# Kernel tuning notes

Measured on AMD Instinct MI355X. Metric: run time of the kernel, lower is better.

The kernel has to match this reference:

```python
import jax, jax.numpy as jnp
import numpy as np

N_USER = 100_000
N_WALLET = 100_000
E = 1_600_000
HID, OUT = 128, 64
H, C = 4, 32  # GAT heads, per-head channels (HID // 4)
U_IN, W_IN = 16, 4
EPS = 1e-5


def _sage(x_src, x_dst, ei, w_l, b_l, w_r):
    """PyG SAGEConv (mean aggr): lin_l(mean_j x_j) + lin_r(x_i)."""
    src, dst = ei[0], ei[1]
    n = x_dst.shape[0]
    s = jax.ops.segment_sum(x_src[src], dst, num_segments=n)
    deg = jax.ops.segment_sum(jnp.ones((src.shape[0],), x_src.dtype), dst, num_segments=n)
    agg = s / jnp.maximum(deg, 1.0)[:, None]
    return agg @ w_l + b_l + x_dst @ w_r


def _bn(x, g, b):
    """BatchNorm over node dim (training-mode batch stats)."""
    m = x.mean(0)
    v = x.var(0)
    return (x - m) * jax.lax.rsqrt(v + EPS) * g + b


def _segment_softmax(logits, seg, n):
    m = jax.ops.segment_max(logits, seg, num_segments=n)
    e = jnp.exp(logits - m[seg])
    s = jax.ops.segment_sum(e, seg, num_segments=n)
    return e / (s[seg] + 1e-16)


def _gat(x, ei, w, a_src, a_dst, bias):
    """PyG GATConv with self-loops, heads concatenated. Dropout off (eval)."""
    n = x.shape[0]
    loop = jnp.arange(n, dtype=ei.dtype)
    src = jnp.concatenate([ei[0], loop])
    dst = jnp.concatenate([ei[1], loop])
    xp = (x @ w).reshape(n, H, C)                      # [n,H,C]
    al_s = (xp * a_src).sum(-1)                        # [n,H]
    al_d = (xp * a_dst).sum(-1)                        # [n,H]
    logits = jax.nn.leaky_relu(al_s[src] + al_d[dst], 0.2)  # [E+n,H]
    alpha = _segment_softmax(logits, dst, n)
    out = jax.ops.segment_sum(xp[src] * alpha[:, :, None], dst, num_segments=n)
    return out.reshape(n, H * C) + bias


def setup_inputs() -> dict:
    key = jax.random.key(0)
    ks = jax.random.split(key, 24)
    rn = lambda k, s, sc=0.05: jax.random.normal(k, s, jnp.float32) * sc
    ei = lambda k, n: jax.random.randint(k, (2, E), 0, n, jnp.int32)
    return {
        "x_user": rn(ks[0], (N_USER, U_IN), 1.0),
        "x_wallet": rn(ks[1], (N_WALLET, W_IN), 1.0),
        "w_u2w_l": rn(ks[2], (U_IN, HID)), "b_u2w": jnp.zeros((HID,), jnp.float32), "w_u2w_r": rn(ks[3], (W_IN, HID)),
        "w_w2u_l": rn(ks[4], (W_IN, HID)), "b_w2u": jnp.zeros((HID,), jnp.float32), "w_w2u_r": rn(ks[5], (U_IN, HID)),
        "w_u2u_l": rn(ks[6], (U_IN, HID)), "b_u2u": jnp.zeros((HID,), jnp.float32), "w_u2u_r": rn(ks[7], (U_IN, HID)),
        "bn_u_g": jnp.ones((HID,), jnp.float32), "bn_u_b": jnp.zeros((HID,), jnp.float32),
        "bn_w_g": jnp.ones((HID,), jnp.float32), "bn_w_b": jnp.zeros((HID,), jnp.float32),
        "gat_w": rn(ks[8], (HID, H * C)), "gat_as": rn(ks[9], (H, C)), "gat_ad": rn(ks[10], (H, C)),
        "gat_b": jnp.zeros((HID,), jnp.float32),
        "bn2_g": jnp.ones((HID,), jnp.float32), "bn2_b": jnp.zeros((HID,), jnp.float32),
        "proj_w": rn(ks[11], (HID, OUT)), "proj_b": jnp.zeros((OUT,), jnp.float32),
        "ei_uw": ei(ks[12], N_USER),   # src user -> dst wallet (both 100k)
        "ei_wu": ei(ks[13], N_WALLET),  # src wallet -> dst user
        "ei_uu": ei(ks[14], N_USER),
    }


def reference(x_user, x_wallet, w_u2w_l, b_u2w, w_u2w_r, w_w2u_l, b_w2u, w_w2u_r,
              w_u2u_l, b_u2u, w_u2u_r, bn_u_g, bn_u_b, bn_w_g, bn_w_b,
              gat_w, gat_as, gat_ad, gat_b, bn2_g, bn2_b, proj_w, proj_b,
              ei_uw, ei_wu, ei_uu):
    h_w_from_u = jax.nn.relu(_sage(x_user, x_wallet, ei_uw, w_u2w_l, b_u2w, w_u2w_r))
    h_u_from_w = jax.nn.relu(_sage(x_wallet, x_user, ei_wu, w_w2u_l, b_w2u, w_w2u_r))
    h_u_from_u = jax.nn.relu(_sage(x_user, x_user, ei_uu, w_u2u_l, b_u2u, w_u2u_r))
    h_user = _bn(h_u_from_w + h_u_from_u, bn_u_g, bn_u_b)
    _ = _bn(h_w_from_u, bn_w_g, bn_w_b)  # h_wallet: computed in torch module but unused in output
    h_user = jax.nn.relu(_gat(h_user, ei_uu, gat_w, gat_as, gat_ad, gat_b))
    h_user = _bn(h_user, bn2_g, bn2_b)
    return jax.nn.relu(h_user @ proj_w + proj_b)  # dropout = identity (eval)
```

## Files before the change

### kernel.cpp

```cpp
#include <hip/hip_runtime.h>
#include <hip/hip_bf16.h>
#include <cstdint>
#include <cstddef>

#define NN   100000
#define NE   1600000
#define CAP  48

#define NBKT 784
#define BSH  7
#define FB   16
#define BCAP 2432
#define ACHUNK 8192
#define NABLK 196

#define NTILES 1563
#define CH_BN 50
#define NSHAD 4
#define LOG2E 1.44269504088896f

typedef __attribute__((ext_vector_type(8))) short short8;
typedef __attribute__((ext_vector_type(4))) float floatx4;

__device__ inline short f2bs(float x) {
    __hip_bfloat16 h = __float2bfloat16(x);
    return *reinterpret_cast<short*>(&h);
}
__device__ inline int pack2(float a, float b) {
    return ((int)(unsigned short)f2bs(b) << 16) | (unsigned short)f2bs(a);
}
__device__ inline float bflo(unsigned p) { return __uint_as_float(p << 16); }
__device__ inline float bfhi(unsigned p) { return __uint_as_float(p & 0xFFFF0000u); }

#define OFF_PRE   ((size_t)0)
#define OFF_BKTU  ((size_t)0)
#define OFF_BKTW  ((size_t)1906688)
#define OFF_XP    ((size_t)12800000)
#define OFF_AGGU  ((size_t)12800000)
#define OFF_AGGW  ((size_t)14400000)
#define OFF_COLU  ((size_t)19200000)
#define OFF_S1    ((size_t)24000000)
#define OFF_Q1    ((size_t)24000512)
#define OFF_S2    ((size_t)24001024)
#define OFF_Q2    ((size_t)24001536)
#define OFF_BCUR  ((size_t)24002048)
#define OFF_CNTU  ((size_t)25600000)
#define OFF_ALS   ((size_t)25802112)
#define OFF_ALD   ((size_t)26202112)
#define ZBASE     OFF_S1
#define ZFLOATS   ((size_t)3648)

__global__ void __launch_bounds__(256) bin_edges(
    const int* __restrict__ ei_u, const int* __restrict__ ei_w,
    int* __restrict__ bcur_u, int* __restrict__ bkt_u,
    int* __restrict__ bcur_w, int* __restrict__ bkt_w) {
    const int* ei = blockIdx.y ? ei_w : ei_u;
    int* bcur = blockIdx.y ? bcur_w : bcur_u;
    int* bkt  = blockIdx.y ? bkt_w  : bkt_u;
    __shared__ int lcnt[NBKT];
    __shared__ int lbuf[NBKT * FB];
    for (int i = threadIdx.x; i < NBKT; i += 256) lcnt[i] = 0;
    __syncthreads();
    int base = blockIdx.x * ACHUNK;
    #pragma unroll 4
    for (int k = 0; k < ACHUNK / 256; k++) {
        int e = base + k * 256 + threadIdx.x;
        if (e < NE) {
            int src = ei[e], dst = ei[NE + e];
            int b = dst >> BSH;
            int pk = ((dst & ((1 << BSH) - 1)) << 17) | src;
            int pos = atomicAdd(&lcnt[b], 1);
            if (pos < FB) lbuf[b * FB + pos] = pk;
            else {
                int g = atomicAdd(&bcur[b], 1);
                if (g < BCAP) bkt[(size_t)b * BCAP + g] = pk;
            }
        }
    }
    __syncthreads();
    int wid = threadIdx.x >> 6, lane = threadIdx.x & 63;
    const int BPW = NBKT / 4;
    int b0w = wid * BPW;
    for (int r = 0; r < BPW; r += 64) {
        int rb = r + lane;
        if (rb < BPW) {
            int b = b0w + rb;
            int c = lcnt[b];
            int nn2 = c < FB ? c : FB;
            if (nn2 > 0) {
                int g0 = atomicAdd(&bcur[b], nn2);
                for (int i2 = 0; i2 < nn2; i2++) {
                    int g = g0 + i2;
                    if (g < BCAP) bkt[(size_t)b * BCAP + g] = lbuf[b * FB + i2];
                }
            }
        }
    }
}

__global__ void __launch_bounds__(256) csr_agg(
    const int* __restrict__ bcur_u, const int* __restrict__ bkt_u,
    int* __restrict__ cnt_g, int* __restrict__ col_g,
    const float* __restrict__ xu, float* __restrict__ aggu,
    const int* __restrict__ bcur_w, const int* __restrict__ bkt_w,
    const float* __restrict__ xw, float* __restrict__ aggw) {
    int type = blockIdx.y;
    const int* bcur = type ? bcur_w : bcur_u;
    const int* bkt  = type ? bkt_w  : bkt_u;
    int B = blockIdx.x;
    int node_base = B << BSH;
    if (node_base >= NN) return;
    __shared__ int cnt[128];
    __shared__ int col[128 * CAP];
    if (threadIdx.x < 128) cnt[threadIdx.x] = 0;
    __syncthreads();
    int n = bcur[B]; if (n > BCAP) n = BCAP;
    const int* bp = bkt + (size_t)B * BCAP;
    for (int i = threadIdx.x; i < n; i += 256) {
        int p = bp[i];
        int d = p >> 17;
        int pos = atomicAdd(&cnt[d], 1);
        if (pos < CAP) col[d * CAP + pos] = p & 0x1FFFF;
    }
    __syncthreads();
    int nn_here = NN - node_base; if (nn_here > 128) nn_here = 128;
    int wv = threadIdx.x >> 6, lane = threadIdx.x & 63;

    if (type == 0) {
        if (threadIdx.x < nn_here) cnt_g[node_base + threadIdx.x] = cnt[threadIdx.x];
        int total4 = nn_here * CAP / 4;
        const int4* cs = (const int4*)col;
        int4* cg = (int4*)(col_g + (size_t)node_base * CAP);
        for (int i = threadIdx.x; i < total4; i += 256) cg[i] = cs[i];
        int kq = lane & 3, nd = (lane >> 2) & 3, sl = lane >> 4;
        const float4* xu4 = (const float4*)xu;
        for (int nb = wv * 32; nb < wv * 32 + 32; nb += 4) {
            int myn = nb + nd;
            int deg = cnt[myn];
            int nu = deg < CAP ? deg : CAP;
            int numax = nu;
            numax = max(numax, __shfl_xor(numax, 4, 64));
            numax = max(numax, __shfl_xor(numax, 8, 64));
            int iters2 = (numax + 7) >> 3;
            float4 v = make_float4(0.f, 0.f, 0.f, 0.f);
            for (int it = 0; it < iters2; it++) {
                int b0 = sl + (it << 3);
                int b1 = b0 + 4;
                int s0 = (b0 < nu) ? col[myn * CAP + b0] : 0;
                int s1 = (b1 < nu) ? col[myn * CAP + b1] : 0;
                float4 x0 = xu4[(size_t)s0 * 4 + kq];
                float4 x1 = xu4[(size_t)s1 * 4 + kq];
                if (b0 < nu) { v.x += x0.x; v.y += x0.y; v.z += x0.z; v.w += x0.w; }
                if (b1 < nu) { v.x += x1.x; v.y += x1.y; v.z += x1.z; v.w += x1.w; }
            }
            v.x += __shfl_xor(v.x, 16, 64); v.y += __shfl_xor(v.y, 16, 64);
            v.z += __shfl_xor(v.z, 16, 64); v.w += __shfl_xor(v.w, 16, 64);
            v.x += __shfl_xor(v.x, 32, 64); v.y += __shfl_xor(v.y, 32, 64);
            v.z += __shfl_xor(v.z, 32, 64); v.w += __shfl_xor(v.w, 32, 64);
            if (lane < 16) {
                int wn = nb + (lane >> 2);
                if (wn < nn_here) {
                    float r = 1.f / fmaxf((float)cnt[wn], 1.f);
                    float4 o = make_float4(v.x * r, v.y * r, v.z * r, v.w * r);
                    *(float4*)&aggu[(size_t)(node_base + wn) * 16 + 4 * (lane & 3)] = o;
                }
            }
        }
    } else {
        const float4* xw4 = (const float4*)xw;
        for (int nl = wv * 32; nl < wv * 32 + 32; nl += 2) {
            if (nl >= nn_here) break;
            int degA = cnt[nl];
            int degB = (nl + 1 < nn_here) ? cnt[nl + 1] : 0;
            int nwA = degA < CAP ? degA : CAP;
            int nwB = degB < CAP ? degB : CAP;
            int sA = (lane < nwA) ? col[nl * CAP + lane] : 0;
            int sB = (lane < nwB) ? col[(nl + 1) * CAP + lane] : 0;
            float4 xA = xw4[sA];
            float4 xB = xw4[sB];
            float4 vA = (lane < nwA) ? xA : make_float4(0.f, 0.f, 0.f, 0.f);
            float4 vB = (lane < nwB) ? xB : make_float4(0.f, 0.f, 0.f, 0.f);
            #pragma unroll
            for (int m = 1; m <= 32; m <<= 1) {
                vA.x += __shfl_xor(vA.x, m, 64); vA.y += __shfl_xor(vA.y, m, 64);
                vA.z += __shfl_xor(vA.z, m, 64); vA.w += __shfl_xor(vA.w, m, 64);
                vB.x += __shfl_xor(vB.x, m, 64); vB.y += __shfl_xor(vB.y, m, 64);
                vB.z += __shfl_xor(vB.z, m, 64); vB.w += __shfl_xor(vB.w, m, 64);
            }
            if (lane == 0) {
                float rA = 1.f / fmaxf((float)degA, 1.f);
                float4 oA = make_float4(vA.x * rA, vA.y * rA, vA.z * rA, vA.w * rA);
                *(float4*)&aggw[(size_t)(node_base + nl) * 4] = oA;
                if (nl + 1 < nn_here) {
                    float rB = 1.f / fmaxf((float)degB, 1.f);
                    float4 oB = make_float4(vB.x * rB, vB.y * rB, vB.z * rB, vB.w * rB);
                    *(float4*)&aggw[(size_t)(node_base + nl + 1) * 4] = oB;
                }
            }
        }
    }
}

__global__ void __launch_bounds__(256, 2) sage_gemm(
    const float* __restrict__ aggu, const float* __restrict__ aggw,
    const float* __restrict__ xu,
    const float* __restrict__ wl_w2u, const float* __restrict__ b_w2u, const float* __restrict__ wr_w2u,
    const float* __restrict__ wl_u2u, const float* __restrict__ b_u2u, const float* __restrict__ wr_u2u,
    __hip_bfloat16* __restrict__ pre,
    float* __restrict__ bnsum, float* __restrict__ bnsq) {
    __shared__ short lw[16 * 64 * 8];
    __shared__ short la[64 * 136];
    __shared__ float lbs[128], lbq[128];
    int tid = threadIdx.x;
    for (int idx = tid; idx < 8192; idx += 256) {
        int mat = idx >> 12;
        int k = (idx >> 7) & 31, n = idx & 127;
        float w;
        if (mat == 0)
            w = (k < 4) ? wl_w2u[k * 128 + n] : (k < 20 ? wr_w2u[(k - 4) * 128 + n] : 0.f);
        else
            w = (k < 16) ? wl_u2u[k * 128 + n] : wr_u2u[(k - 16) * 128 + n];
        int t = n >> 4, l15 = n & 15, q = (k >> 3) & 3, j = k & 7;
        lw[((mat * 8 + t) * 64 + q * 16 + l15) * 8 + j] = f2bs(w);
    }
    if (tid < 128) { lbs[tid] = 0.f; lbq[tid] = 0.f; }
    __syncthreads();
    int wv = tid >> 6, lane = tid & 63;
    int quad = lane >> 4, l15 = lane & 15;
    short8 w1[8], w2[8];
    #pragma unroll
    for (int t = 0; t < 8; t++) {
        w1[t] = *(const short8*)&lw[(t * 64 + lane) * 8];
        w2[t] = *(const short8*)&lw[((8 + t) * 64 + lane) * 8];
    }
    float bw[8], bu[8];
    #pragma unroll
    for (int t = 0; t < 8; t++) {
        bw[t] = b_w2u[t * 16 + l15];
        bu[t] = b_u2u[t * 16 + l15];
    }
    float sE[8], qE[8];
    #pragma unroll
    for (int t = 0; t < 8; t++) { sE[t] = 0.f; qE[t] = 0.f; }
    for (int tile = blockIdx.x; tile < NTILES; tile += gridDim.x) {
        int nbase = tile * 64;
        __syncthreads();
        {
            int node = tid >> 2, p = tid & 3;
            int gn = nbase + node;
            float4 v = make_float4(0.f, 0.f, 0.f, 0.f);
            if (gn < NN) v = *(const float4*)&xu[(size_t)gn * 16 + 4 * p];
            int2 pk; pk.x = pack2(v.x, v.y); pk.y = pack2(v.z, v.w);
            *(int2*)&la[node * 136 + 4 + 4 * p] = pk;
            *(int2*)&la[node * 136 + 48 + 4 * p] = pk;
        }
        {
            int node = tid >> 2, p = tid & 3;
            int gn = nbase + node;
            float4 v = make_float4(0.f, 0.f, 0.f, 0.f);
            if (gn < NN) v = *(const float4*)&aggu[(size_t)gn * 16 + 4 * p];
            int2 pk; pk.x = pack2(v.x, v.y); pk.y = pack2(v.z, v.w);
            *(int2*)&la[node * 136 + 32 + 4 * p] = pk;
        }
        if (tid < 64) {
            int node = tid, gn = nbase + node;
            float4 v = make_float4(0.f, 0.f, 0.f, 0.f);
            if (gn < NN) v = *(const float4*)&aggw[(size_t)gn * 4];
            int2 pk; pk.x = pack2(v.x, v.y); pk.y = pack2(v.z, v.w);
            *(int2*)&la[node * 136 + 0] = pk;
            int2 z; z.x = 0; z.y = 0;
            *(int2*)&la[node * 136 + 20] = z;
            *(int2*)&la[node * 136 + 24] = z;
            *(int2*)&la[node * 136 + 28] = z;
        }
        __syncthreads();
        short8 af1 = *(const short8*)&la[(wv * 16 + l15) * 136 + quad * 8];
        short8 af2 = *(const short8*)&la[(wv * 16 + l15) * 136 + 32 + quad * 8];
        floatx4 acc1[8], acc2[8];
        #pragma unroll
        for (int t = 0; t < 8; t++) {
            acc1[t] = (floatx4){0.f, 0.f, 0.f, 0.f};
            acc2[t] = (floatx4){0.f, 0.f, 0.f, 0.f};
        }
        #pragma unroll
        for (int t = 0; t < 8; t++) {
            acc1[t] = __builtin_amdgcn_mfma_f32_16x16x32_bf16(af1, w1[t], acc1[t], 0, 0, 0);
            acc2[t] = __builtin_amdgcn_mfma_f32_16x16x32_bf16(af2, w2[t], acc2[t], 0, 0, 0);
        }
        __syncthreads();
        #pragma unroll
        for (int t = 0; t < 8; t++)
            #pragma unroll
            for (int r = 0; r < 4; r++) {
                float v1 = fmaxf(acc1[t][r] + bw[t], 0.f);
                float v2 = fmaxf(acc2[t][r] + bu[t], 0.f);
                short vv = f2bs(v1 + v2);
                la[(wv * 16 + quad * 4 + r) * 136 + t * 16 + l15] = vv;
                int node = nbase + wv * 16 + quad * 4 + r;
                if (node < NN) {
                    float vr = __uint_as_float(((unsigned)(unsigned short)vv) << 16);
                    sE[t] += vr; qE[t] += vr * vr;
                }
            }
        __syncthreads();
        #pragma unroll
        for (int c = 0; c < 4; c++) {
            int idx = c * 256 + tid;
            int node = idx >> 4, f8 = (idx & 15) * 8;
            int gn = nbase + node;
            if (gn < NN)
                *(int4*)(pre + (size_t)gn * 128 + f8) = *(const int4*)&la[node * 136 + f8];
        }
    }
    __syncthreads();
    #pragma unroll
    for (int t = 0; t < 8; t++) {
        atomicAdd(&lbs[t * 16 + l15], sE[t]);
        atomicAdd(&lbq[t * 16 + l15], qE[t]);
    }
    __syncthreads();
    if (tid < 128) {
        int sh = (blockIdx.x & (NSHAD - 1)) << 7;
        atomicAdd(&bnsum[sh + tid], lbs[tid]);
        atomicAdd(&bnsq[sh + tid], lbq[tid]);
    }
}

__global__ void __launch_bounds__(256) bn_stats_act2(const unsigned* __restrict__ x2,
                                                     const float* __restrict__ gb,
                                                     float* __restrict__ sum, float* __restrict__ sq) {
    int f2 = threadIdx.x & 63, half = threadIdx.x >> 6;
    int n0 = blockIdx.x * CH_BN;
    float gb0 = gb[2 * f2], gb1 = gb[2 * f2 + 1];
    float s0 = 0.f, q0 = 0.f, s1 = 0.f, q1 = 0.f;
    for (int i = n0 + half; i < n0 + CH_BN; i += 4) {
        unsigned p = x2[(size_t)i * 64 + f2];
        float v0 = fmaxf(bflo(p) + gb0, 0.f), v1 = fmaxf(bfhi(p) + gb1, 0.f);
        s0 += v0; q0 += v0 * v0; s1 += v1; q1 += v1 * v1;
    }
    __shared__ float a0[256], c0[256], a1[256], c1[256];
    a0[threadIdx.x] = s0; c0[threadIdx.x] = q0;
    a1[threadIdx.x] = s1; c1[threadIdx.x] = q1;
    __syncthreads();
    if (half == 0) {
        for (int h = 1; h < 4; h++) {
            s0 += a0[h * 64 + f2]; q0 += c0[h * 64 + f2];
            s1 += a1[h * 64 + f2]; q1 += c1[h * 64 + f2];
        }
        int sh = (blockIdx.x & (NSHAD - 1)) << 7;
        atomicAdd(&sum[sh + 2 * f2], s0);     atomicAdd(&sq[sh + 2 * f2], q0);
        atomicAdd(&sum[sh + 2 * f2 + 1], s1); atomicAdd(&sq[sh + 2 * f2 + 1], q1);
    }
}

__global__ void __launch_bounds__(256, 2) gemm_al(
    const unsigned* __restrict__ pre2, const float* __restrict__ s1, const float* __restrict__ q1,
    const float* __restrict__ bng, const float* __restrict__ bnb,
    const float* __restrict__ gw, const float* __restrict__ gas, const float* __restrict__ gad,
    __hip_bfloat16* __restrict__ xp, float* __restrict__ al_s, float* __restrict__ al_d) {
    __shared__ short lw[32 * 64 * 8];
    __shared__ short la[64 * 136];
    __shared__ float lsc[128], lsh[128];
    int tid = threadIdx.x;
    if (tid < 128) {
        float sv = s1[tid] + s1[128 + tid] + s1[256 + tid] + s1[384 + tid];
        float qv = q1[tid] + q1[128 + tid] + q1[256 + tid] + q1[384 + tid];
        float m = sv * (1.0f / NN);
        float v = qv * (1.0f / NN) - m * m;
        float sc = bng[tid] * rsqrtf(v + 1e-5f);
        lsc[tid] = sc; lsh[tid] = bnb[tid] - m * sc;
    }
    for (int idx = tid; idx < 16384; idx += 256) {
        int k = idx >> 7, n = idx & 127;
        int t = n >> 4, l15 = n & 15, s = k >> 5, q = (k >> 3) & 3, j = k & 7;
        lw[(((t * 4 + s) * 64) + q * 16 + l15) * 8 + j] = f2bs(gw[idx]);
    }
    __syncthreads();
    int wv = tid >> 6, lane = tid & 63;
    int quad = lane >> 4, l15 = lane & 15;
    short8 wfrag[8][4];
    #pragma unroll
    for (int t = 0; t < 8; t++)
        #pragma unroll
        for (int s = 0; s < 4; s++)
            wfrag[t][s] = *(const short8*)&lw[((t * 4 + s) * 64 + lane) * 8];
    float asv[8], adv[8];
    #pragma unroll
    for (int t = 0; t < 8; t++) {
        asv[t] = gas[t * 16 + l15] * LOG2E;
        adv[t] = gad[t * 16 + l15] * LOG2E;
    }
    for (int tile = blockIdx.x; tile < NTILES; tile += gridDim.x) {
        int nbase = tile * 64;
        __syncthreads();
        #pragma unroll
        for (int c = 0; c < 8; c++) {
            int idx = c * 256 + tid;
            int node = idx >> 5, g = idx & 31;
            uint2 pp = make_uint2(0u, 0u);
            int gn = nbase + node;
            if (gn < NN) pp = *(const uint2*)&pre2[(size_t)gn * 64 + 2 * g];
            int f = 4 * g;
            float v0 = bflo(pp.x), v1 = bfhi(pp.x), v2 = bflo(pp.y), v3 = bfhi(pp.y);
            int2 pk;
            pk.x = pack2(v0 * lsc[f] + lsh[f],         v1 * lsc[f + 1] + lsh[f + 1]);
            pk.y = pack2(v2 * lsc[f + 2] + lsh[f + 2], v3 * lsc[f + 3] + lsh[f + 3]);
            *(int2*)&la[node * 136 + f] = pk;
        }
        __syncthreads();
        short8 af[4];
        #pragma unroll
        for (int s = 0; s < 4; s++)
            af[s] = *(const short8*)&la[(wv * 16 + l15) * 136 + s * 32 + quad * 8];
        floatx4 acc[8];
        #pragma unroll
        for (int t = 0; t < 8; t++) acc[t] = (floatx4){0.f, 0.f, 0.f, 0.f};
        #pragma unroll
        for (int s = 0; s < 4; s++)
            #pragma unroll
            for (int t = 0; t < 8; t++)
                acc[t] = __builtin_amdgcn_mfma_f32_16x16x32_bf16(af[s], wfrag[t][s], acc[t], 0, 0, 0);
        #pragma unroll
        for (int r = 0; r < 4; r++) {
            int node = nbase + wv * 16 + quad * 4 + r;
            #pragma unroll
            for (int h = 0; h < 4; h++) {
                float vs = acc[2 * h][r] * asv[2 * h] + acc[2 * h + 1][r] * asv[2 * h + 1];
                float vd = acc[2 * h][r] * adv[2 * h] + acc[2 * h + 1][r] * adv[2 * h + 1];
                #pragma unroll
                for (int m = 8; m >= 1; m >>= 1) {
                    vs += __shfl_xor(vs, m, 64);
                    vd += __shfl_xor(vd, m, 64);
                }
                if (l15 == 0 && node < NN) {
                    al_s[(size_t)node * 4 + h] = vs;
                    al_d[(size_t)node * 4 + h] = vd;
                }
            }
        }
        __syncthreads();
        #pragma unroll
        for (int t = 0; t < 8; t++)
            #pragma unroll
            for (int r = 0; r < 4; r++)
                la[(wv * 16 + quad * 4 + r) * 136 + t * 16 + l15] = f2bs(acc[t][r]);
        __syncthreads();
        #pragma unroll
        for (int c = 0; c < 4; c++) {
            int idx = c * 256 + tid;
            int node = idx >> 4, f8 = (idx & 15) * 8;
            int gn = nbase + node;
            if (gn < NN)
                *(int4*)(xp + (size_t)gn * 128 + f8) = *(const int4*)&la[node * 136 + f8];
        }
    }
}

__global__ void __launch_bounds__(256, 2) gemm_proj(
    const unsigned* __restrict__ gat2, const float* __restrict__ gb,
    const float* __restrict__ s2, const float* __restrict__ q2,
    const float* __restrict__ bng, const float* __restrict__ bnb,
    const float* __restrict__ pw, const float* __restrict__ pb,
    float* __restrict__ out) {
    __shared__ short lw[16 * 64 * 8];
    __shared__ short la[64 * 136];
    __shared__ float lsc[128], lsh[128], lgb[128];
    int tid = threadIdx.x;
    if (tid < 128) {
        float sv = s2[tid] + s2[128 + tid] + s2[256 + tid] + s2[384 + tid];
        float qv = q2[tid] + q2[128 + tid] + q2[256 + tid] + q2[384 + tid];
        float m = sv * (1.0f / NN);
        float v = qv * (1.0f / NN) - m * m;
        float sc = bng[tid] * rsqrtf(v + 1e-5f);
        lsc[tid] = sc; lsh[tid] = bnb[tid] - m * sc;
        lgb[tid] = gb[tid];
    }
    for (int idx = tid; idx < 8192; idx += 256) {
        int k = idx >> 6, n = idx & 63;
        int t = n >> 4, l15 = n & 15, s = k >> 5, q = (k >> 3) & 3, j = k & 7;
        lw[(((t * 4 + s) * 64) + q * 16 + l15) * 8 + j] = f2bs(pw[idx]);
    }
    __syncthreads();
    int wv = tid >> 6, lane = tid & 63;
    int quad = lane >> 4, l15 = lane & 15;
    short8 wfrag[4][4];
    #pragma unroll
    for (int t = 0; t < 4; t++)
        #pragma unroll
        for (int s = 0; s < 4; s++)
            wfrag[t][s] = *(const short8*)&lw[((t * 4 + s) * 64 + lane) * 8];
    float pbv[4];
    #pragma unroll
    for (int t = 0; t < 4; t++) pbv[t] = pb[t * 16 + l15];
    for (int tile = blockIdx.x; tile < NTILES; tile += gridDim.x) {
        int nbase = tile * 64;
        __syncthreads();
        #pragma unroll
        for (int c = 0; c < 8; c++) {
            int idx = c * 256 + tid;
            int node = idx >> 5, g = idx & 31;
            uint2 pp = make_uint2(0u, 0u);
            int gn = nbase + node;
            if (gn < NN) pp = *(const uint2*)&gat2[(size_t)gn * 64 + 2 * g];
            int f = 4 * g;
            float h0 = fmaxf(bflo(pp.x) + lgb[f],     0.f) * lsc[f]     + lsh[f];
            float h1 = fmaxf(bfhi(pp.x) + lgb[f + 1], 0.f) * lsc[f + 1] + lsh[f + 1];
            float h2 = fmaxf(bflo(pp.y) + lgb[f + 2], 0.f) * lsc[f + 2] + lsh[f + 2];
            float h3 = fmaxf(bfhi(pp.y) + lgb[f + 3], 0.f) * lsc[f + 3] + lsh[f + 3];
            int2 pk; pk.x = pack2(h0, h1); pk.y = pack2(h2, h3);
            *(int2*)&la[node * 136 + f] = pk;
        }
        __syncthreads();
        short8 af[4];
        #pragma unroll
        for (int s = 0; s < 4; s++)
            af[s] = *(const short8*)&la[(wv * 16 + l15) * 136 + s * 32 + quad * 8];
        floatx4 acc[4];
        #pragma unroll
        for (int t = 0; t < 4; t++) acc[t] = (floatx4){0.f, 0.f, 0.f, 0.f};
        #pragma unroll
        for (int s = 0; s < 4; s++)
            #pragma unroll
            for (int t = 0; t < 4; t++)
                acc[t] = __builtin_amdgcn_mfma_f32_16x16x32_bf16(af[s], wfrag[t][s], acc[t], 0, 0, 0);
        #pragma unroll
        for (int r = 0; r < 4; r++) {
            int gn = nbase + wv * 16 + quad * 4 + r;
            if (gn < NN) {
                #pragma unroll
                for (int t = 0; t < 4; t++)
                    out[(size_t)gn * 64 + t * 16 + l15] = fmaxf(acc[t][r] + pbv[t], 0.f);
            }
        }
    }
}

__global__ void __launch_bounds__(256) gat_gather(
    const int* __restrict__ cnt_u, const int* __restrict__ col_u,
    const float* __restrict__ al_s, const float* __restrict__ al_d,
    const unsigned* __restrict__ xp2, unsigned* __restrict__ gout2) {
    int i = (blockIdx.x * 256 + threadIdx.x) >> 6;
    int lane = threadIdx.x & 63;
    int g = lane >> 4, q = lane & 15;
    int h = q >> 2;
    float ad = al_d[(size_t)i * 4 + h];
    int deg = cnt_u[i];
    int n = deg < CAP ? deg : CAP;
    int mycol = (lane < n) ? col_u[(size_t)i * CAP + lane] : 0;
    float a0 = 0.f, a1 = 0.f, a2 = 0.f, a3 = 0.f;
    float a4 = 0.f, a5 = 0.f, a6 = 0.f, a7 = 0.f, den = 0.f;
    if (g == 0) {
        float l = al_s[(size_t)i * 4 + h] + ad;
        float e = exp2f(fmaxf(l, 0.2f * l));
        uint4 p = *(const uint4*)&xp2[(size_t)i * 64 + 4 * q];
        a0 = e * bflo(p.x); a1 = e * bfhi(p.x);
        a2 = e * bflo(p.y); a3 = e * bfhi(p.y);
        a4 = e * bflo(p.z); a5 = e * bfhi(p.z);
        a6 = e * bflo(p.w); a7 = e * bfhi(p.w);
        den = e;
    }
    for (int b = 0; b < n; b += 16) {
        int s[4]; float A[4]; uint4 p[4];
        #pragma unroll
        for (int u = 0; u < 4; u++)
            s[u] = __shfl(mycol, b + 4 * u + g, 64);
        #pragma unroll
        for (int u = 0; u < 4; u++)
            A[u] = al_s[(size_t)s[u] * 4 + h];
        #pragma unroll
        for (int u = 0; u < 4; u++)
            p[u] = *(const uint4*)&xp2[(size_t)s[u] * 64 + 4 * q];
        #pragma unroll
        for (int u = 0; u < 4; u++) {
            float l = A[u] + ad;
            float e = (b + 4 * u + g < n) ? exp2f(fmaxf(l, 0.2f * l)) : 0.f;
            a0 += e * bflo(p[u].x); a1 += e * bfhi(p[u].x);
            a2 += e * bflo(p[u].y); a3 += e * bfhi(p[u].y);
            a4 += e * bflo(p[u].z); a5 += e * bfhi(p[u].z);
            a6 += e * bflo(p[u].w); a7 += e * bfhi(p[u].w);
            den += e;
        }
    }
    a0 += __shfl_xor(a0, 16, 64); a0 += __shfl_xor(a0, 32, 64);
    a1 += __shfl_xor(a1, 16, 64); a1 += __shfl_xor(a1, 32, 64);
    a2 += __shfl_xor(a2, 16, 64); a2 += __shfl_xor(a2, 32, 64);
    a3 += __shfl_xor(a3, 16, 64); a3 += __shfl_xor(a3, 32, 64);
    a4 += __shfl_xor(a4, 16, 64); a4 += __shfl_xor(a4, 32, 64);
    a5 += __shfl_xor(a5, 16, 64); a5 += __shfl_xor(a5, 32, 64);
    a6 += __shfl_xor(a6, 16, 64); a6 += __shfl_xor(a6, 32, 64);
    a7 += __shfl_xor(a7, 16, 64); a7 += __shfl_xor(a7, 32, 64);
    den += __shfl_xor(den, 16, 64); den += __shfl_xor(den, 32, 64);
    if (g == 0) {
        float r = 1.0f / (den + 1e-16f);
        uint4 o;
        o.x = (unsigned)pack2(a0 * r, a1 * r);
        o.y = (unsigned)pack2(a2 * r, a3 * r);
        o.z = (unsigned)pack2(a4 * r, a5 * r);
        o.w = (unsigned)pack2(a6 * r, a7 * r);
        *(uint4*)&gout2[(size_t)i * 64 + 4 * q] = o;
    }
}

extern "C" void kernel_launch(void* const* d_in, const int* in_sizes, int n_in,
                              void* d_out, int out_size, void* d_ws, size_t ws_size,
                              hipStream_t stream) {
    const float* x_user   = (const float*)d_in[0];
    const float* x_wallet = (const float*)d_in[1];
    const float* w_w2u_l  = (const float*)d_in[5];
    const float* b_w2u    = (const float*)d_in[6];
    const float* w_w2u_r  = (const float*)d_in[7];
    const float* w_u2u_l  = (const float*)d_in[8];
    const float* b_u2u    = (const float*)d_in[9];
    const float* w_u2u_r  = (const float*)d_in[10];
    const float* bn_u_g   = (const float*)d_in[11];
    const float* bn_u_b   = (const float*)d_in[12];
    const float* gat_w    = (const float*)d_in[15];
    const float* gat_as   = (const float*)d_in[16];
    const float* gat_ad   = (const float*)d_in[17];
    const float* gat_b    = (const float*)d_in[18];
    const float* bn2_g    = (const float*)d_in[19];
    const float* bn2_b    = (const float*)d_in[20];
    const float* proj_w   = (const float*)d_in[21];
    const float* proj_b   = (const float*)d_in[22];
    const int* ei_wu      = (const int*)d_in[24];
    const int* ei_uu      = (const int*)d_in[25];
    float* out = (float*)d_out;
    float* ws  = (float*)d_ws;

    unsigned* pre2 = (unsigned*)(ws + OFF_PRE);
    __hip_bfloat16* pre = (__hip_bfloat16*)(ws + OFF_PRE);
    int*   bkt_u  = (int*)(ws + OFF_BKTU);
    int*   bkt_w  = (int*)(ws + OFF_BKTW);
    __hip_bfloat16* xp = (__hip_bfloat16*)(ws + OFF_XP);
    unsigned* xp2 = (unsigned*)(ws + OFF_XP);
    float* aggu = ws + OFF_AGGU;
    float* aggw = ws + OFF_AGGW;
    int*   col_u  = (int*)(ws + OFF_COLU);
    int*   cnt_u  = (int*)(ws + OFF_CNTU);
    int*   bcur_u = (int*)(ws + OFF_BCUR);
    int*   bcur_w = (int*)(ws + OFF_BCUR) + 800;
    float* al_s = ws + OFF_ALS, *al_d = ws + OFF_ALD;
    float* s1 = ws + OFF_S1, *q1 = ws + OFF_Q1;
    float* s2 = ws + OFF_S2, *q2 = ws + OFF_Q2;

    hipMemsetAsync(ws + ZBASE, 0, ZFLOATS * sizeof(float), stream);

    bin_edges<<<dim3(NABLK, 2), 256, 0, stream>>>(ei_uu, ei_wu, bcur_u, bkt_u, bcur_w, bkt_w);

    csr_agg<<<dim3(NBKT, 2), 256, 0, stream>>>(
        bcur_u, bkt_u, cnt_u, col_u, x_user, aggu,
        bcur_w, bkt_w, x_wallet, aggw);

    sage_gemm<<<512, 256, 0, stream>>>(
        aggu, aggw, x_user, w_w2u_l, b_w2u, w_w2u_r, w_u2u_l, b_u2u, w_u2u_r,
        pre, s1, q1);

    gemm_al<<<512, 256, 0, stream>>>(pre2, s1, q1, bn_u_g, bn_u_b,
                                     gat_w, gat_as, gat_ad, xp, al_s, al_d);

    unsigned* gat2 = pre2;
    gat_gather<<<NN / 4, 256, 0, stream>>>(cnt_u, col_u, al_s, al_d, xp2, gat2);

    bn_stats_act2<<<NN / CH_BN, 256, 0, stream>>>(gat2, gat_b, s2, q2);

    gemm_proj<<<512, 256, 0, stream>>>(gat2, gat_b, s2, q2, bn2_g, bn2_b,
                                       proj_w, proj_b, out);
}
```

Before: 408.3 us.

## Fuse second BatchNorm statistics into GAT gather with persistent grid-stride blocks

Removes the separate bn_stats_act2 pass by accumulating per-feature sum and sum-of-squares of relu(gat+bias) inside gat_gather, which becomes a persistent kernel with 2048 blocks striding over nodes. Partial sums are reduced in shared memory and then atomically added into 64 shadow copies, which gemm_proj sums when it computes the BN scale. This saves one full read of the 25.6 MB GAT output and one kernel launch. In exchange the gather runs with fewer blocks and so less latency hiding, and the statistics are taken from the bf16-rounded values, as before.

```diff
diff --git a/kernel.cpp b/kernel.cpp
--- a/kernel.cpp
+++ b/kernel.cpp
@@ -15,9 +15,12 @@
 #define NABLK 196
 
 #define NTILES 1563
-#define CH_BN 50
 #define NSHAD 4
+#define NSH2  64
 #define LOG2E 1.44269504088896f
+
+#define GGBLK 2048
+#define NWAVE (GGBLK * 4)
 
 typedef __attribute__((ext_vector_type(8))) short short8;
 typedef __attribute__((ext_vector_type(4))) float floatx4;
@@ -42,13 +45,13 @@
 #define OFF_S1    ((size_t)24000000)
 #define OFF_Q1    ((size_t)24000512)
 #define OFF_S2    ((size_t)24001024)
-#define OFF_Q2    ((size_t)24001536)
-#define OFF_BCUR  ((size_t)24002048)
+#define OFF_Q2    ((size_t)24009216)
+#define OFF_BCUR  ((size_t)24017408)
 #define OFF_CNTU  ((size_t)25600000)
 #define OFF_ALS   ((size_t)25802112)
 #define OFF_ALD   ((size_t)26202112)
 #define ZBASE     OFF_S1
-#define ZFLOATS   ((size_t)3648)
+#define ZFLOATS   ((size_t)19008)
 
 __global__ void __launch_bounds__(256) bin_edges(
     const int* __restrict__ ei_u, const int* __restrict__ ei_w,
@@ -326,33 +329,6 @@
     }
 }
 
-__global__ void __launch_bounds__(256) bn_stats_act2(const unsigned* __restrict__ x2,
-                                                     const float* __restrict__ gb,
-                                                     float* __restrict__ sum, float* __restrict__ sq) {
-    int f2 = threadIdx.x & 63, half = threadIdx.x >> 6;
-    int n0 = blockIdx.x * CH_BN;
-    float gb0 = gb[2 * f2], gb1 = gb[2 * f2 + 1];
-    float s0 = 0.f, q0 = 0.f, s1 = 0.f, q1 = 0.f;
-    for (int i = n0 + half; i < n0 + CH_BN; i += 4) {
-        unsigned p = x2[(size_t)i * 64 + f2];
-        float v0 = fmaxf(bflo(p) + gb0, 0.f), v1 = fmaxf(bfhi(p) + gb1, 0.f);
-        s0 += v0; q0 += v0 * v0; s1 += v1; q1 += v1 * v1;
-    }
-    __shared__ float a0[256], c0[256], a1[256], c1[256];
-    a0[threadIdx.x] = s0; c0[threadIdx.x] = q0;
-    a1[threadIdx.x] = s1; c1[threadIdx.x] = q1;
-    __syncthreads();
-    if (half == 0) {
-        for (int h = 1; h < 4; h++) {
-            s0 += a0[h * 64 + f2]; q0 += c0[h * 64 + f2];
-            s1 += a1[h * 64 + f2]; q1 += c1[h * 64 + f2];
-        }
-        int sh = (blockIdx.x & (NSHAD - 1)) << 7;
-        atomicAdd(&sum[sh + 2 * f2], s0);     atomicAdd(&sq[sh + 2 * f2], q0);
-        atomicAdd(&sum[sh + 2 * f2 + 1], s1); atomicAdd(&sq[sh + 2 * f2 + 1], q1);
-    }
-}
-
 __global__ void __launch_bounds__(256, 2) gemm_al(
     const unsigned* __restrict__ pre2, const float* __restrict__ s1, const float* __restrict__ q1,
     const float* __restrict__ bng, const float* __restrict__ bnb,
@@ -467,8 +443,11 @@
     __shared__ float lsc[128], lsh[128], lgb[128];
     int tid = threadIdx.x;
     if (tid < 128) {
-        float sv = s2[tid] + s2[128 + tid] + s2[256 + tid] + s2[384 + tid];
-        float qv = q2[tid] + q2[128 + tid] + q2[256 + tid] + q2[384 + tid];
+        float sv = 0.f, qv = 0.f;
+        for (int s = 0; s < NSH2; s++) {
+            sv += s2[s * 128 + tid];
+            qv += q2[s * 128 + tid];
+        }
         float m = sv * (1.0f / NN);
         float v = qv * (1.0f / NN) - m * m;
         float sc = bng[tid] * rsqrtf(v + 1e-5f);
@@ -538,66 +517,101 @@
 __global__ void __launch_bounds__(256) gat_gather(
     const int* __restrict__ cnt_u, const int* __restrict__ col_u,
     const float* __restrict__ al_s, const float* __restrict__ al_d,
-    const unsigned* __restrict__ xp2, unsigned* __restrict__ gout2) {
-    int i = (blockIdx.x * 256 + threadIdx.x) >> 6;
-    int lane = threadIdx.x & 63;
+    const unsigned* __restrict__ xp2, unsigned* __restrict__ gout2,
+    const float* __restrict__ gb, float* __restrict__ s2g, float* __restrict__ q2g) {
+    __shared__ float lss[128], lqq[128];
+    int tid = threadIdx.x;
+    int wv = tid >> 6, lane = tid & 63;
     int g = lane >> 4, q = lane & 15;
     int h = q >> 2;
-    float ad = al_d[(size_t)i * 4 + h];
-    int deg = cnt_u[i];
-    int n = deg < CAP ? deg : CAP;
-    int mycol = (lane < n) ? col_u[(size_t)i * CAP + lane] : 0;
-    float a0 = 0.f, a1 = 0.f, a2 = 0.f, a3 = 0.f;
-    float a4 = 0.f, a5 = 0.f, a6 = 0.f, a7 = 0.f, den = 0.f;
+    if (tid < 128) { lss[tid] = 0.f; lqq[tid] = 0.f; }
+    float gbv[8];
+    #pragma unroll
+    for (int j = 0; j < 8; j += 4)
+        *(float4*)&gbv[j] = *(const float4*)&gb[8 * q + j];
+    float sE[8], qE[8];
+    #pragma unroll
+    for (int j = 0; j < 8; j++) { sE[j] = 0.f; qE[j] = 0.f; }
+
+    for (int i = blockIdx.x * 4 + wv; i < NN; i += NWAVE) {
+        float ad = al_d[(size_t)i * 4 + h];
+        int deg = cnt_u[i];
+        int n = deg < CAP ? deg : CAP;
+        int mycol = (lane < n) ? col_u[(size_t)i * CAP + lane] : 0;
+        float a0 = 0.f, a1 = 0.f, a2 = 0.f, a3 = 0.f;
+        float a4 = 0.f, a5 = 0.f, a6 = 0.f, a7 = 0.f, den = 0.f;
+        if (g == 0) {
+            float l = al_s[(size_t)i * 4 + h] + ad;
+            float e = exp2f(fmaxf(l, 0.2f * l));
+            uint4 p = *(const uint4*)&xp2[(size_t)i * 64 + 4 * q];
+            a0 = e * bflo(p.x); a1 = e * bfhi(p.x);
+            a2 = e * bflo(p.y); a3 = e * bfhi(p.y);
+            a4 = e * bflo(p.z); a5 = e * bfhi(p.z);
+            a6 = e * bflo(p.w); a7 = e * bfhi(p.w);
+            den = e;
+        }
+        for (int b = 0; b < n; b += 16) {
+            int s[4]; float A[4]; uint4 p[4];
+            #pragma unroll
+            for (int u = 0; u < 4; u++)
+                s[u] = __shfl(mycol, b + 4 * u + g, 64);
+            #pragma unroll
+            for (int u = 0; u < 4; u++)
+                A[u] = al_s[(size_t)s[u] * 4 + h];
+            #pragma unroll
+            for (int u = 0; u < 4; u++)
+                p[u] = *(const uint4*)&xp2[(size_t)s[u] * 64 + 4 * q];
+            #pragma unroll
+            for (int u = 0; u < 4; u++) {
+                float l = A[u] + ad;
+                float e = (b + 4 * u + g < n) ? exp2f(fmaxf(l, 0.2f * l)) : 0.f;
+                a0 += e * bflo(p[u].x); a1 += e * bfhi(p[u].x);
+                a2 += e * bflo(p[u].y); a3 += e * bfhi(p[u].y);
+                a4 += e * bflo(p[u].z); a5 += e * bfhi(p[u].z);
+                a6 += e * bflo(p[u].w); a7 += e * bfhi(p[u].w);
+                den += e;
+            }
+        }
+        a0 += __shfl_xor(a0, 16, 64); a0 += __shfl_xor(a0, 32, 64);
+        a1 += __shfl_xor(a1, 16, 64); a1 += __shfl_xor(a1, 32, 64);
+        a2 += __shfl_xor(a2, 16, 64); a2 += __shfl_xor(a2, 32, 64);
+        a3 += __shfl_xor(a3, 16, 64); a3 += __shfl_xor(a3, 32, 64);
+        a4 += __shfl_xor(a4, 16, 64); a4 += __shfl_xor(a4, 32, 64);
+        a5 += __shfl_xor(a5, 16, 64); a5 += __shfl_xor(a5, 32, 64);
+        a6 += __shfl_xor(a6, 16, 64); a6 += __shfl_xor(a6, 32, 64);
+        a7 += __shfl_xor(a7, 16, 64); a7 += __shfl_xor(a7, 32, 64);
+        den += __shfl_xor(den, 16, 64); den += __shfl_xor(den, 32, 64);
+        if (g == 0) {
+            float r = 1.0f / (den + 1e-16f);
+            uint4 o;
+            o.x = (unsigned)pack2(a0 * r, a1 * r);
+            o.y = (unsigned)pack2(a2 * r, a3 * r);
+            o.z = (unsigned)pack2(a4 * r, a5 * r);
+            o.w = (unsigned)pack2(a6 * r, a7 * r);
+            *(uint4*)&gout2[(size_t)i * 64 + 4 * q] = o;
+            float vv0 = fmaxf(bflo(o.x) + gbv[0], 0.f), vv1 = fmaxf(bfhi(o.x) + gbv[1], 0.f);
+            float vv2 = fmaxf(bflo(o.y) + gbv[2], 0.f), vv3 = fmaxf(bfhi(o.y) + gbv[3], 0.f);
+            float vv4 = fmaxf(bflo(o.z) + gbv[4], 0.f), vv5 = fmaxf(bfhi(o.z) + gbv[5], 0.f);
+            float vv6 = fmaxf(bflo(o.w) + gbv[6], 0.f), vv7 = fmaxf(bfhi(o.w) + gbv[7], 0.f);
+            sE[0] += vv0; qE[0] += vv0 * vv0;  sE[1] += vv1; qE[1] += vv1 * vv1;
+            sE[2] += vv2; qE[2] += vv2 * vv2;  sE[3] += vv3; qE[3] += vv3 * vv3;
+            sE[4] += vv4; qE[4] += vv4 * vv4;  sE[5] += vv5; qE[5] += vv5 * vv5;
+            sE[6] += vv6; qE[6] += vv6 * vv6;  sE[7] += vv7; qE[7] += vv7 * vv7;
+        }
+    }
+    __syncthreads();
     if (g == 0) {
-        float l = al_s[(size_t)i * 4 + h] + ad;
-        float e = exp2f(fmaxf(l, 0.2f * l));
-        uint4 p = *(const uint4*)&xp2[(size_t)i * 64 + 4 * q];
-        a0 = e * bflo(p.x); a1 = e * bfhi(p.x);
-        a2 = e * bflo(p.y); a3 = e * bfhi(p.y);
-        a4 = e * bflo(p.z); a5 = e * bfhi(p.z);
-        a6 = e * bflo(p.w); a7 = e * bfhi(p.w);
-        den = e;
-    }
-    for (int b = 0; b < n; b += 16) {
-        int s[4]; float A[4]; uint4 p[4];
-        #pragma unroll
-        for (int u = 0; u < 4; u++)
-            s[u] = __shfl(mycol, b + 4 * u + g, 64);
-        #pragma unroll
-        for (int u = 0; u < 4; u++)
-            A[u] = al_s[(size_t)s[u] * 4 + h];
-        #pragma unroll
-        for (int u = 0; u < 4; u++)
-            p[u] = *(const uint4*)&xp2[(size_t)s[u] * 64 + 4 * q];
-        #pragma unroll
-        for (int u = 0; u < 4; u++) {
-            float l = A[u] + ad;
-            float e = (b + 4 * u + g < n) ? exp2f(fmaxf(l, 0.2f * l)) : 0.f;
-            a0 += e * bflo(p[u].x); a1 += e * bfhi(p[u].x);
-            a2 += e * bflo(p[u].y); a3 += e * bfhi(p[u].y);
-            a4 += e * bflo(p[u].z); a5 += e * bfhi(p[u].z);
-            a6 += e * bflo(p[u].w); a7 += e * bfhi(p[u].w);
-            den += e;
-        }
-    }
-    a0 += __shfl_xor(a0, 16, 64); a0 += __shfl_xor(a0, 32, 64);
-    a1 += __shfl_xor(a1, 16, 64); a1 += __shfl_xor(a1, 32, 64);
-    a2 += __shfl_xor(a2, 16, 64); a2 += __shfl_xor(a2, 32, 64);
-    a3 += __shfl_xor(a3, 16, 64); a3 += __shfl_xor(a3, 32, 64);
-    a4 += __shfl_xor(a4, 16, 64); a4 += __shfl_xor(a4, 32, 64);
-    a5 += __shfl_xor(a5, 16, 64); a5 += __shfl_xor(a5, 32, 64);
-    a6 += __shfl_xor(a6, 16, 64); a6 += __shfl_xor(a6, 32, 64);
-    a7 += __shfl_xor(a7, 16, 64); a7 += __shfl_xor(a7, 32, 64);
-    den += __shfl_xor(den, 16, 64); den += __shfl_xor(den, 32, 64);
-    if (g == 0) {
-        float r = 1.0f / (den + 1e-16f);
-        uint4 o;
-        o.x = (unsigned)pack2(a0 * r, a1 * r);
-        o.y = (unsigned)pack2(a2 * r, a3 * r);
-        o.z = (unsigned)pack2(a4 * r, a5 * r);
-        o.w = (unsigned)pack2(a6 * r, a7 * r);
-        *(uint4*)&gout2[(size_t)i * 64 + 4 * q] = o;
+        #pragma unroll
+        for (int j = 0; j < 8; j++) {
+            atomicAdd(&lss[8 * q + j], sE[j]);
+            atomicAdd(&lqq[8 * q + j], qE[j]);
+        }
+    }
+    __syncthreads();
+    if (tid < 128) {
+        int sh = (blockIdx.x & (NSH2 - 1)) << 7;
+        atomicAdd(&s2g[sh + tid], lss[tid]);
+        atomicAdd(&q2g[sh + tid], lqq[tid]);
     }
 }
 
@@ -659,9 +673,8 @@
                                      gat_w, gat_as, gat_ad, xp, al_s, al_d);
 
     unsigned* gat2 = pre2;
-    gat_gather<<<NN / 4, 256, 0, stream>>>(cnt_u, col_u, al_s, al_d, xp2, gat2);
-
-    bn_stats_act2<<<NN / CH_BN, 256, 0, stream>>>(gat2, gat_b, s2, q2);
+    gat_gather<<<GGBLK, 256, 0, stream>>>(cnt_u, col_u, al_s, al_d, xp2, gat2,
+                                          gat_b, s2, q2);
 
     gemm_proj<<<512, 256, 0, stream>>>(gat2, gat_b, s2, q2, bn2_g, bn2_b,
                                        proj_w, proj_b, out);
```

Measured after the change: 402.2 us (median of 3 runs). Within noise of the previous version (-1.5%).
